# Performance work log

Hardware: AMD Instinct MI355X
Metric: run time of the kernel (lower is better)

The kernel has to match this reference:

```python
import jax, jax.numpy as jnp
import numpy as np

N = 100000
E = 1600000
F_IN = 128
F_OUT = 128
BN_EPS = 1e-5


def setup_inputs() -> dict:
    key = jax.random.key(0)
    ks = jax.random.split(key, 8)
    x = jax.random.normal(ks[0], (N, F_IN), dtype=jnp.float32)
    edge_index = jax.random.randint(ks[1], (2, E), 0, N, dtype=jnp.int64)
    s1 = 1.0 / np.sqrt(F_IN)
    s2 = 1.0 / np.sqrt(F_OUT)
    W1 = jax.random.uniform(ks[2], (F_OUT, F_IN), jnp.float32, -s1, s1)
    b1 = jax.random.uniform(ks[3], (F_OUT,), jnp.float32, -s1, s1)
    gamma = jnp.ones((F_OUT,), jnp.float32)
    beta = jnp.zeros((F_OUT,), jnp.float32)
    W2 = jax.random.uniform(ks[4], (F_OUT, F_OUT), jnp.float32, -s2, s2)
    b2 = jax.random.uniform(ks[5], (F_OUT,), jnp.float32, -s2, s2)
    eps = jnp.zeros((1,), jnp.float32)
    return {"x": x, "edge_index": edge_index, "eps": eps, "W1": W1, "b1": b1,
            "gamma": gamma, "beta": beta, "W2": W2, "b2": b2}


def reference(x, edge_index, eps, W1, b1, gamma, beta, W2, b2):
    row, col = edge_index[0], edge_index[1]
    # gather neighbor features then scatter-add by destination node
    neighbor_sum = jax.ops.segment_sum(x[col], row, num_segments=x.shape[0])
    out = (1.0 + eps) * x + neighbor_sum  # [N, F_IN]
    h = out @ W1.T + b1                   # [N, F_OUT]
    # BatchNorm1d in training mode: biased batch statistics over nodes
    mean = jnp.mean(h, axis=0)
    var = jnp.mean(jnp.square(h - mean), axis=0)
    h = (h - mean) * jax.lax.rsqrt(var + BN_EPS) * gamma + beta
    h = jax.nn.relu(h)
    return h @ W2.T + b2
```

## Files before the change

kernel.cpp:

```cpp
#include <hip/hip_runtime.h>
#include <hip/hip_bf16.h>

#define NF 128

typedef __attribute__((ext_vector_type(8))) short short8;
typedef __attribute__((ext_vector_type(4))) float f32x4;

__device__ __forceinline__ ushort f2bf(float f) {
    union { __hip_bfloat16 h; ushort u; } c;
    c.h = __float2bfloat16(f);
    return c.u;
}
__device__ __forceinline__ float bf_lo(uint u) { return __uint_as_float(u << 16); }
__device__ __forceinline__ float bf_hi(uint u) { return __uint_as_float(u & 0xffff0000u); }

#define EPB 4096
#define CAP 12800


__global__ void cvtsort_kernel(const float* __restrict__ x, const float* __restrict__ W1,
                               const float* __restrict__ W2, ushort* __restrict__ xb,
                               ushort* __restrict__ W1b, ushort* __restrict__ W2b,
                               const int* __restrict__ ei, int* __restrict__ binOff,
                               uint* __restrict__ pairS, int nx4, int nblkC, int E) {
    __shared__ uint sorted[EPB];
    __shared__ uchar binOf[EPB];
    __shared__ int lcnt[256];
    __shared__ int lofs[256];
    __shared__ int lcur[256];
    __shared__ int gdelta[256];
    __shared__ int wsum[4];
    int t = threadIdx.x;
    int blk = blockIdx.x;
    if (blk < nblkC) {
        lcnt[t] = 0;
        lcur[t] = 0;
        __syncthreads();
        int base = blk * EPB;
        int bn[EPB / 256];
        uint pk[EPB / 256];
#pragma unroll
        for (int it = 0; it < EPB / 256; it++) {
            int e = base + it * 256 + t;
            bn[it] = -1;
            pk[it] = 0;
            if (e < E) {
                int r = ei[e];
                int c = ei[E + e];
                bn[it] = r >> 9;
                pk[it] = ((uint)(r & 511) << 17) | (uint)c;
                atomicAdd(&lcnt[bn[it]], 1);
            }
        }
        __syncthreads();
        int v = lcnt[t];
        int lane = t & 63, w = t >> 6;
        int sv = v;
#pragma unroll
        for (int d = 1; d < 64; d <<= 1) {
            int n = __shfl_up(sv, d, 64);
            if (lane >= d) sv += n;
        }
        if (lane == 63) wsum[w] = sv;
        __syncthreads();
        int wpre = 0;
#pragma unroll
        for (int i = 0; i < 3; i++)
            if (i < w) wpre += wsum[i];
        int myOfs = sv + wpre - v;
        int g = v ? atomicAdd(&binOff[t], v) : 0;
        lofs[t] = myOfs;
        gdelta[t] = t * CAP + g - myOfs;
        __syncthreads();
#pragma unroll
        for (int it = 0; it < EPB / 256; it++) {
            if (bn[it] >= 0) {
                int b = bn[it];
                int p = lofs[b] + atomicAdd(&lcur[b], 1);
                sorted[p] = pk[it];
                binOf[p] = (uchar)b;
            }
        }
        __syncthreads();
        int nvalid = min(EPB, E - base);
        for (int i = t; i < nvalid; i += 256)
            pairS[gdelta[binOf[i]] + i] = sorted[i];
    }
    int gid = blk * 256 + t;
    const float* src;
    ushort* dst;
    int idx;
    if (gid < nx4) { src = x; dst = xb; idx = gid; }
    else if (gid < nx4 + 4096) { src = W1; dst = W1b; idx = gid - nx4; }
    else if (gid < nx4 + 8192) { src = W2; dst = W2b; idx = gid - nx4 - 4096; }
    else return;
    float4 v = reinterpret_cast<const float4*>(src)[idx];
    ushort4 o;
    o.x = f2bf(v.x); o.y = f2bf(v.y); o.z = f2bf(v.z); o.w = f2bf(v.w);
    reinterpret_cast<ushort4*>(dst)[idx] = o;
}

__global__ void passDE_kernel(const uint* __restrict__ pairS, const int* __restrict__ binOff,
                              int* __restrict__ rowptr, int* __restrict__ adj, int N, int E) {
    __shared__ int hist[512];
    __shared__ int cur[512];
    __shared__ int wsum[4];
    __shared__ int sBase;
    int t = threadIdx.x;
    int b = blockIdx.x;
    hist[t] = 0;
    hist[t + 256] = 0;
    if (t < 64) {
        int acc = 0;
        for (int i = t; i < b; i += 64) acc += binOff[i];
#pragma unroll
        for (int d = 32; d > 0; d >>= 1) acc += __shfl_xor(acc, d, 64);
        if (t == 0) sBase = acc;
    }
    __syncthreads();
    int base = sBase;
    int cnt = binOff[b];
    size_t pbase = (size_t)b * CAP;
    for (int i = t; i < cnt; i += 256)
        atomicAdd(&hist[pairS[pbase + i] >> 17], 1);
    __syncthreads();
    int h0 = hist[2 * t], h1 = hist[2 * t + 1];
    int v = h0 + h1;
    int lane = t & 63, w = t >> 6;
    int sv = v;
#pragma unroll
    for (int d = 1; d < 64; d <<= 1) {
        int n = __shfl_up(sv, d, 64);
        if (lane >= d) sv += n;
    }
    if (lane == 63) wsum[w] = sv;
    __syncthreads();
    int wpre = 0;
#pragma unroll
    for (int i = 0; i < 3; i++)
        if (i < w) wpre += wsum[i];
    int e0 = base + sv + wpre - v;
    int e1 = e0 + h0;
    int g0 = b * 512 + 2 * t;
    if (g0 < N) rowptr[g0] = e0;
    if (g0 + 1 < N) rowptr[g0 + 1] = e1;
    if (t == 0 && b == gridDim.x - 1) rowptr[N] = E;
    cur[2 * t] = e0;
    cur[2 * t + 1] = e1;
    __syncthreads();
    for (int i = t; i < cnt; i += 256) {
        uint p = pairS[pbase + i];
        int slot = atomicAdd(&cur[p >> 17], 1);
        adj[slot] = (int)(p & 0x1FFFF);
    }
}

#define ACCV(v)                                                   \
    a0 += bf_lo((v).x); a1 += bf_hi((v).x);                       \
    a2 += bf_lo((v).y); a3 += bf_hi((v).y);                       \
    a4 += bf_lo((v).z); a5 += bf_hi((v).z);                       \
    a6 += bf_lo((v).w); a7 += bf_hi((v).w);

__global__ void gather_kernel(const uint4* __restrict__ xb4, const int* __restrict__ rowptr,
                              const int* __restrict__ adj, const float* __restrict__ eps,
                              uint4* __restrict__ aggb4, int N) {
    int t = blockIdx.x * blockDim.x + threadIdx.x;
    int node = t >> 4;
    int lane = t & 15;
    if (node >= N) return;
    uint4 u = xb4[(size_t)node * 16 + lane];
    float s = 1.0f + eps[0];
    float a0 = bf_lo(u.x) * s, a1 = bf_hi(u.x) * s;
    float a2 = bf_lo(u.y) * s, a3 = bf_hi(u.y) * s;
    float a4 = bf_lo(u.z) * s, a5 = bf_hi(u.z) * s;
    float a6 = bf_lo(u.w) * s, a7 = bf_hi(u.w) * s;
    int j = rowptr[node], end = rowptr[node + 1];
    for (; j + 8 <= end; j += 8) {
        int c0 = adj[j],     c1 = adj[j + 1], c2 = adj[j + 2], c3 = adj[j + 3];
        int c4 = adj[j + 4], c5 = adj[j + 5], c6 = adj[j + 6], c7 = adj[j + 7];
        uint4 v0 = xb4[(size_t)c0 * 16 + lane];
        uint4 v1 = xb4[(size_t)c1 * 16 + lane];
        uint4 v2 = xb4[(size_t)c2 * 16 + lane];
        uint4 v3 = xb4[(size_t)c3 * 16 + lane];
        uint4 v4 = xb4[(size_t)c4 * 16 + lane];
        uint4 v5 = xb4[(size_t)c5 * 16 + lane];
        uint4 v6 = xb4[(size_t)c6 * 16 + lane];
        uint4 v7 = xb4[(size_t)c7 * 16 + lane];
        ACCV(v0) ACCV(v1) ACCV(v2) ACCV(v3)
        ACCV(v4) ACCV(v5) ACCV(v6) ACCV(v7)
    }
    if (j + 4 <= end) {
        int c0 = adj[j], c1 = adj[j + 1], c2 = adj[j + 2], c3 = adj[j + 3];
        uint4 v0 = xb4[(size_t)c0 * 16 + lane];
        uint4 v1 = xb4[(size_t)c1 * 16 + lane];
        uint4 v2 = xb4[(size_t)c2 * 16 + lane];
        uint4 v3 = xb4[(size_t)c3 * 16 + lane];
        ACCV(v0) ACCV(v1) ACCV(v2) ACCV(v3)
        j += 4;
    }
    if (j + 2 <= end) {
        int c0 = adj[j], c1 = adj[j + 1];
        uint4 v0 = xb4[(size_t)c0 * 16 + lane];
        uint4 v1 = xb4[(size_t)c1 * 16 + lane];
        ACCV(v0) ACCV(v1)
        j += 2;
    }
    if (j < end) {
        uint4 v0 = xb4[(size_t)adj[j] * 16 + lane];
        ACCV(v0)
    }
    uint4 o;
    o.x = (uint)f2bf(a0) | ((uint)f2bf(a1) << 16);
    o.y = (uint)f2bf(a2) | ((uint)f2bf(a3) << 16);
    o.z = (uint)f2bf(a4) | ((uint)f2bf(a5) << 16);
    o.w = (uint)f2bf(a6) | ((uint)f2bf(a7) << 16);
    aggb4[(size_t)node * 16 + lane] = o;
}

template <int MODE>
__global__ __launch_bounds__(256) void mgemm_kernel(
    const ushort* __restrict__ Ab, const ushort* __restrict__ Wb,
    const float* __restrict__ bias, float* __restrict__ out,
    ushort* __restrict__ hb, float* __restrict__ stats,
    const float* __restrict__ gamma, const float* __restrict__ beta, int N) {
    __shared__ __align__(16) ushort smem[2 * 128 * 136];
    __shared__ float redS[256];
    __shared__ float redQ[256];
    __shared__ float scL[128];
    __shared__ float shL[128];
    ushort* As = smem;
    ushort* Bs = smem + 128 * 136;

    const int t = threadIdx.x;
    const int row0 = blockIdx.x * 128;
    const int r16 = t >> 4;
    const int c8 = (t & 15) * 8;

    if (MODE == 1 && t < 128) {
        float inv_n = 1.0f / (float)N;
        float mean = stats[t] * inv_n;
        float var = fmaxf(stats[128 + t] * inv_n - mean * mean, 0.0f);
        float s = gamma[t] * rsqrtf(var + 1e-5f);
        scL[t] = s;
        shL[t] = beta[t] - mean * s;
    }
    if (MODE == 1) __syncthreads();

    float sc[8], sh[8];
    if (MODE == 1) {
#pragma unroll
        for (int i = 0; i < 8; i++) { sc[i] = scL[c8 + i]; sh[i] = shL[c8 + i]; }
    }

#pragma unroll
    for (int it = 0; it < 8; it++) {
        int row = it * 16 + r16;
        int gr = row0 + row;
        if (MODE == 0) {
            uint4 v = make_uint4(0, 0, 0, 0);
            if (gr < N) v = *reinterpret_cast<const uint4*>(Ab + (size_t)gr * NF + c8);
            *reinterpret_cast<uint4*>(&As[row * 136 + c8]) = v;
        } else {
            uint4 v = make_uint4(0, 0, 0, 0);
            if (gr < N) v = *reinterpret_cast<const uint4*>(hb + (size_t)gr * NF + c8);
            float vv[8] = {bf_lo(v.x), bf_hi(v.x), bf_lo(v.y), bf_hi(v.y),
                           bf_lo(v.z), bf_hi(v.z), bf_lo(v.w), bf_hi(v.w)};
#pragma unroll
            for (int i = 0; i < 8; i++) vv[i] = fmaxf(vv[i] * sc[i] + sh[i], 0.0f);
            uint4 p;
            p.x = (uint)f2bf(vv[0]) | ((uint)f2bf(vv[1]) << 16);
            p.y = (uint)f2bf(vv[2]) | ((uint)f2bf(vv[3]) << 16);
            p.z = (uint)f2bf(vv[4]) | ((uint)f2bf(vv[5]) << 16);
            p.w = (uint)f2bf(vv[6]) | ((uint)f2bf(vv[7]) << 16);
            *reinterpret_cast<uint4*>(&As[row * 136 + c8]) = p;
        }
        uint4 w = *reinterpret_cast<const uint4*>(Wb + row * NF + c8);
        *reinterpret_cast<uint4*>(&Bs[row * 136 + c8]) = w;
    }
    __syncthreads();

    const int wid = t >> 6;
    const int lane = t & 63;
    const int quad = lane >> 4;
    const int l16 = lane & 15;
    const int wm = wid >> 1;
    const int wn = wid & 1;

    f32x4 acc[4][4];
#pragma unroll
    for (int tm = 0; tm < 4; tm++)
#pragma unroll
        for (int tn = 0; tn < 4; tn++) acc[tm][tn] = (f32x4)(0.0f);

#pragma unroll
    for (int ks = 0; ks < 4; ks++) {
        short8 a[4], b[4];
#pragma unroll
        for (int tm = 0; tm < 4; tm++)
            a[tm] = *reinterpret_cast<const short8*>(
                &As[(wm * 64 + tm * 16 + l16) * 136 + ks * 32 + quad * 8]);
#pragma unroll
        for (int tn = 0; tn < 4; tn++)
            b[tn] = *reinterpret_cast<const short8*>(
                &Bs[(wn * 64 + tn * 16 + l16) * 136 + ks * 32 + quad * 8]);
#pragma unroll
        for (int tm = 0; tm < 4; tm++)
#pragma unroll
            for (int tn = 0; tn < 4; tn++)
                acc[tm][tn] = __builtin_amdgcn_mfma_f32_16x16x32_bf16(a[tm], b[tn],
                                                                      acc[tm][tn], 0, 0, 0);
    }

    float bs[4];
#pragma unroll
    for (int tn = 0; tn < 4; tn++) bs[tn] = bias[wn * 64 + tn * 16 + l16];

    __syncthreads();
    ushort* htile = As;
    float* ftile = reinterpret_cast<float*>(smem);

    float ssum[4] = {0.f, 0.f, 0.f, 0.f}, sq[4] = {0.f, 0.f, 0.f, 0.f};
#pragma unroll
    for (int tm = 0; tm < 4; tm++) {
        int rb = wm * 64 + tm * 16 + quad * 4;
#pragma unroll
        for (int reg = 0; reg < 4; reg++) {
            int gr = row0 + rb + reg;
            bool ok = gr < N;
#pragma unroll
            for (int tn = 0; tn < 4; tn++) {
                int col = wn * 64 + tn * 16 + l16;
                float h = acc[tm][tn][reg] + bs[tn];
                if (MODE == 0) {
                    htile[(rb + reg) * 128 + col] = f2bf(h);
                    if (ok) { ssum[tn] += h; sq[tn] += h * h; }
                } else {
                    ftile[(rb + reg) * 128 + col] = h;
                }
            }
        }
    }
    __syncthreads();

    if (MODE == 0) {
        for (int i = t; i < 2048; i += 256) {
            int row = i >> 4;
            int gr = row0 + row;
            if (gr < N)
                *reinterpret_cast<uint4*>(hb + (size_t)gr * NF + (i & 15) * 8) =
                    *reinterpret_cast<const uint4*>(htile + row * 128 + (i & 15) * 8);
        }
    } else {
        for (int i = t; i < 4096; i += 256) {
            int row = i >> 5;
            int gr = row0 + row;
            if (gr < N)
                *reinterpret_cast<float4*>(out + (size_t)gr * NF + (i & 31) * 4) =
                    *reinterpret_cast<const float4*>(ftile + row * 128 + (i & 31) * 4);
        }
    }

    if (MODE == 0) {
#pragma unroll
        for (int tn = 0; tn < 4; tn++) {
            float s = ssum[tn], q = sq[tn];
            s += __shfl_xor(s, 16); s += __shfl_xor(s, 32);
            q += __shfl_xor(q, 16); q += __shfl_xor(q, 32);
            if (quad == 0) {
                int c = wn * 64 + tn * 16 + l16;
                redS[wm * 128 + c] = s;
                redQ[wm * 128 + c] = q;
            }
        }
        __syncthreads();
        if (t < 128) {
            unsafeAtomicAdd(&stats[t], redS[t] + redS[128 + t]);
            unsafeAtomicAdd(&stats[128 + t], redQ[t] + redQ[128 + t]);
        }
    }
}

extern "C" void kernel_launch(void* const* d_in, const int* in_sizes, int n_in,
                              void* d_out, int out_size, void* d_ws, size_t ws_size,
                              hipStream_t stream) {
    const float* x     = (const float*)d_in[0];
    const int* ei      = (const int*)d_in[1];
    const float* eps   = (const float*)d_in[2];
    const float* W1    = (const float*)d_in[3];
    const float* b1    = (const float*)d_in[4];
    const float* gamma = (const float*)d_in[5];
    const float* beta  = (const float*)d_in[6];
    const float* W2    = (const float*)d_in[7];
    const float* b2    = (const float*)d_in[8];
    float* out         = (float*)d_out;

    const int N = in_sizes[0] / NF;
    const int E = in_sizes[1] / 2;

    const int NB = (N + 511) >> 9;
    const int nblkC = (E + EPB - 1) / EPB;

    ushort* xb     = (ushort*)d_ws;
    ushort* aggb   = xb + (size_t)N * NF;
    ushort* W1b    = aggb + (size_t)N * NF;
    ushort* W2b    = W1b + NF * NF;
    float*  stats  = (float*)(W2b + NF * NF);
    int*    binOff = (int*)(stats + 512);
    int*    rowptr = binOff + 256;
    int*    adj    = rowptr + (N + 1);
    uint*   pairS  = (uint*)aggb;
    ushort* hb     = xb;

    (void)hipMemsetAsync(stats, 0, 3072, stream);

    int nx4 = N * 32;
    int cvtBlocks = (nx4 + 8192 + 255) / 256;
    cvtsort_kernel<<<cvtBlocks, 256, 0, stream>>>(x, W1, W2, xb, W1b, W2b, ei, binOff,
                                                  pairS, nx4, nblkC, E);
    passDE_kernel<<<NB, 256, 0, stream>>>(pairS, binOff, rowptr, adj, N, E);

    long long gt = (long long)N * 16;
    gather_kernel<<<(int)((gt + 255) / 256), 256, 0, stream>>>((const uint4*)xb, rowptr, adj,
                                                               eps, (uint4*)aggb, N);

    int gblocks = (N + 127) / 128;
    mgemm_kernel<0><<<gblocks, 256, 0, stream>>>(aggb, W1b, b1, out, hb, stats,
                                                 nullptr, nullptr, N);
    mgemm_kernel<1><<<gblocks, 256, 0, stream>>>(nullptr, W2b, b2, out, hb, stats,
                                                 gamma, beta, N);
}
```

Before: 255.0 us.

## Halve GEMM shared memory by reading weights from global and phasing output

The GEMM kernel no longer stages the weight matrix in LDS. It reads B fragments directly from global memory (cached), and the fp32 output tile is written through LDS in two 64-row phases so only one 128x136 ushort buffer is needed. This cuts LDS per block roughly in half to allow more resident blocks per CU, at the cost of uncoalesced per-lane global weight loads and an extra barrier. The gather kernel is also split into three sequential launches over node ranges, which adds launch overhead without obvious concurrency.

```diff
diff --git a/kernel.cpp b/kernel.cpp
--- a/kernel.cpp
+++ b/kernel.cpp
@@ -163,11 +163,11 @@
 
 __global__ void gather_kernel(const uint4* __restrict__ xb4, const int* __restrict__ rowptr,
                               const int* __restrict__ adj, const float* __restrict__ eps,
-                              uint4* __restrict__ aggb4, int N) {
+                              uint4* __restrict__ aggb4, int node0, int nodeEnd) {
     int t = blockIdx.x * blockDim.x + threadIdx.x;
-    int node = t >> 4;
+    int node = node0 + (t >> 4);
     int lane = t & 15;
-    if (node >= N) return;
+    if (node >= nodeEnd) return;
     uint4 u = xb4[(size_t)node * 16 + lane];
     float s = 1.0f + eps[0];
     float a0 = bf_lo(u.x) * s, a1 = bf_hi(u.x) * s;
@@ -223,13 +223,12 @@
     const float* __restrict__ bias, float* __restrict__ out,
     ushort* __restrict__ hb, float* __restrict__ stats,
     const float* __restrict__ gamma, const float* __restrict__ beta, int N) {
-    __shared__ __align__(16) ushort smem[2 * 128 * 136];
+    __shared__ __align__(16) ushort smem[128 * 136];
     __shared__ float redS[256];
     __shared__ float redQ[256];
     __shared__ float scL[128];
     __shared__ float shL[128];
     ushort* As = smem;
-    ushort* Bs = smem + 128 * 136;
 
     const int t = threadIdx.x;
     const int row0 = blockIdx.x * 128;
@@ -245,12 +244,6 @@
         shL[t] = beta[t] - mean * s;
     }
     if (MODE == 1) __syncthreads();
-
-    float sc[8], sh[8];
-    if (MODE == 1) {
-#pragma unroll
-        for (int i = 0; i < 8; i++) { sc[i] = scL[c8 + i]; sh[i] = shL[c8 + i]; }
-    }
 
 #pragma unroll
     for (int it = 0; it < 8; it++) {
@@ -265,8 +258,11 @@
             if (gr < N) v = *reinterpret_cast<const uint4*>(hb + (size_t)gr * NF + c8);
             float vv[8] = {bf_lo(v.x), bf_hi(v.x), bf_lo(v.y), bf_hi(v.y),
                            bf_lo(v.z), bf_hi(v.z), bf_lo(v.w), bf_hi(v.w)};
-#pragma unroll
-            for (int i = 0; i < 8; i++) vv[i] = fmaxf(vv[i] * sc[i] + sh[i], 0.0f);
+            float sc2[8], sh2[8];
+#pragma unroll
+            for (int i = 0; i < 8; i++) { sc2[i] = scL[c8 + i]; sh2[i] = shL[c8 + i]; }
+#pragma unroll
+            for (int i = 0; i < 8; i++) vv[i] = fmaxf(vv[i] * sc2[i] + sh2[i], 0.0f);
             uint4 p;
             p.x = (uint)f2bf(vv[0]) | ((uint)f2bf(vv[1]) << 16);
             p.y = (uint)f2bf(vv[2]) | ((uint)f2bf(vv[3]) << 16);
@@ -274,8 +270,6 @@
             p.w = (uint)f2bf(vv[6]) | ((uint)f2bf(vv[7]) << 16);
             *reinterpret_cast<uint4*>(&As[row * 136 + c8]) = p;
         }
-        uint4 w = *reinterpret_cast<const uint4*>(Wb + row * NF + c8);
-        *reinterpret_cast<uint4*>(&Bs[row * 136 + c8]) = w;
     }
     __syncthreads();
 
@@ -302,7 +296,7 @@
 #pragma unroll
         for (int tn = 0; tn < 4; tn++)
             b[tn] = *reinterpret_cast<const short8*>(
-                &Bs[(wn * 64 + tn * 16 + l16) * 136 + ks * 32 + quad * 8]);
+                Wb + (wn * 64 + tn * 16 + l16) * NF + ks * 32 + quad * 8);
 #pragma unroll
         for (int tm = 0; tm < 4; tm++)
 #pragma unroll
@@ -316,33 +310,27 @@
     for (int tn = 0; tn < 4; tn++) bs[tn] = bias[wn * 64 + tn * 16 + l16];
 
     __syncthreads();
-    ushort* htile = As;
-    float* ftile = reinterpret_cast<float*>(smem);
-
-    float ssum[4] = {0.f, 0.f, 0.f, 0.f}, sq[4] = {0.f, 0.f, 0.f, 0.f};
-#pragma unroll
-    for (int tm = 0; tm < 4; tm++) {
-        int rb = wm * 64 + tm * 16 + quad * 4;
-#pragma unroll
-        for (int reg = 0; reg < 4; reg++) {
-            int gr = row0 + rb + reg;
-            bool ok = gr < N;
-#pragma unroll
-            for (int tn = 0; tn < 4; tn++) {
-                int col = wn * 64 + tn * 16 + l16;
-                float h = acc[tm][tn][reg] + bs[tn];
-                if (MODE == 0) {
+
+    if (MODE == 0) {
+        ushort* htile = As;
+        float ssum[4] = {0.f, 0.f, 0.f, 0.f}, sq[4] = {0.f, 0.f, 0.f, 0.f};
+#pragma unroll
+        for (int tm = 0; tm < 4; tm++) {
+            int rb = wm * 64 + tm * 16 + quad * 4;
+#pragma unroll
+            for (int reg = 0; reg < 4; reg++) {
+                int gr = row0 + rb + reg;
+                bool ok = gr < N;
+#pragma unroll
+                for (int tn = 0; tn < 4; tn++) {
+                    int col = wn * 64 + tn * 16 + l16;
+                    float h = acc[tm][tn][reg] + bs[tn];
                     htile[(rb + reg) * 128 + col] = f2bf(h);
                     if (ok) { ssum[tn] += h; sq[tn] += h * h; }
-                } else {
-                    ftile[(rb + reg) * 128 + col] = h;
                 }
             }
         }
-    }
-    __syncthreads();
-
-    if (MODE == 0) {
+        __syncthreads();
         for (int i = t; i < 2048; i += 256) {
             int row = i >> 4;
             int gr = row0 + row;
@@ -350,17 +338,6 @@
                 *reinterpret_cast<uint4*>(hb + (size_t)gr * NF + (i & 15) * 8) =
                     *reinterpret_cast<const uint4*>(htile + row * 128 + (i & 15) * 8);
         }
-    } else {
-        for (int i = t; i < 4096; i += 256) {
-            int row = i >> 5;
-            int gr = row0 + row;
-            if (gr < N)
-                *reinterpret_cast<float4*>(out + (size_t)gr * NF + (i & 31) * 4) =
-                    *reinterpret_cast<const float4*>(ftile + row * 128 + (i & 31) * 4);
-        }
-    }
-
-    if (MODE == 0) {
 #pragma unroll
         for (int tn = 0; tn < 4; tn++) {
             float s = ssum[tn], q = sq[tn];
@@ -376,6 +353,34 @@
         if (t < 128) {
             unsafeAtomicAdd(&stats[t], redS[t] + redS[128 + t]);
             unsafeAtomicAdd(&stats[128 + t], redQ[t] + redQ[128 + t]);
+        }
+    } else {
+        float* ftile = reinterpret_cast<float*>(smem);
+#pragma unroll
+        for (int phase = 0; phase < 2; phase++) {
+            if (wm == phase) {
+#pragma unroll
+                for (int tm = 0; tm < 4; tm++) {
+                    int rbl = tm * 16 + quad * 4;
+#pragma unroll
+                    for (int reg = 0; reg < 4; reg++) {
+#pragma unroll
+                        for (int tn = 0; tn < 4; tn++) {
+                            int col = wn * 64 + tn * 16 + l16;
+                            ftile[(rbl + reg) * 128 + col] = acc[tm][tn][reg] + bs[tn];
+                        }
+                    }
+                }
+            }
+            __syncthreads();
+            for (int i = t; i < 2048; i += 256) {
+                int row = phase * 64 + (i >> 5);
+                int gr = row0 + row;
+                if (gr < N)
+                    *reinterpret_cast<float4*>(out + (size_t)gr * NF + (i & 31) * 4) =
+                        *reinterpret_cast<const float4*>(ftile + (i >> 5) * 128 + (i & 31) * 4);
+            }
+            if (phase == 0) __syncthreads();
         }
     }
 }
@@ -419,9 +424,15 @@
                                                   pairS, nx4, nblkC, E);
     passDE_kernel<<<NB, 256, 0, stream>>>(pairS, binOff, rowptr, adj, N, E);
 
-    long long gt = (long long)N * 16;
-    gather_kernel<<<(int)((gt + 255) / 256), 256, 0, stream>>>((const uint4*)xb, rowptr, adj,
-                                                               eps, (uint4*)aggb, N);
+    int third = (N + 2) / 3;
+    for (int s = 0; s < 3; s++) {
+        int n0 = s * third;
+        int n1 = (n0 + third < N) ? n0 + third : N;
+        if (n0 >= n1) break;
+        long long gt = (long long)(n1 - n0) * 16;
+        gather_kernel<<<(int)((gt + 255) / 256), 256, 0, stream>>>(
+            (const uint4*)xb, rowptr, adj, eps, (uint4*)aggb, n0, n1);
+    }
 
     int gblocks = (N + 127) / 128;
     mgemm_kernel<0><<<gblocks, 256, 0, stream>>>(aggb, W1b, b1, out, hb, stats,
```

Result: slower. 272.9 us (+7.0%).
